# Kernel tuning notes

Measured on AMD Instinct MI355X. Metric: run time of the kernel, lower is better.

## Reference

```python
import jax, jax.numpy as jnp
import numpy as np

B, N, FIN, H, D = 4, 2048, 128, 4, 64
ALPHA = 0.2  # LeakyReLU negative slope


def _xavier_uniform(key, shape):
    fan_in, fan_out = shape[0], shape[1]
    limit = float(np.sqrt(6.0 / (fan_in + fan_out)))
    return jax.random.uniform(key, shape, jnp.float32, -limit, limit)


def setup_inputs() -> dict:
    key = jax.random.key(0)
    k1, k2, k3, k4 = jax.random.split(key, 4)
    x = jax.random.normal(k1, (B, N, FIN), jnp.float32)
    adj = jax.random.randint(k2, (B, N, N), 0, 2, jnp.int32)  # dense 0/1 mask
    W = _xavier_uniform(k3, (FIN, H * D))
    a = _xavier_uniform(k4, (2 * D, 1))
    return {"x": x, "adj": adj, "W": W, "a": a}


def reference(x, adj, W, a):
    Bb, Nn, _ = x.shape
    Dd = a.shape[0] // 2
    Hh = W.shape[1] // Dd
    # h: [B, N, H, D]
    h = (x @ W).reshape(Bb, Nn, Hh, Dd)
    # Additive attention: e[b,i,j,h] = leakyrelu(a1 . h[b,i,h] + a2 . h[b,j,h])
    a1 = a[:Dd, 0]
    a2 = a[Dd:, 0]
    ei = jnp.einsum('bnhd,d->bnh', h, a1)  # source (row i) term
    ej = jnp.einsum('bnhd,d->bnh', h, a2)  # dest (col j) term
    e = ei[:, :, None, :] + ej[:, None, :, :]  # [B, N, N, H]
    e = jnp.where(e >= 0, e, ALPHA * e)  # LeakyReLU
    e = jnp.where(adj[..., None] == 0, -jnp.inf, e)
    att = jax.nn.softmax(e, axis=2)  # softmax over neighbors j
    # dropout is a no-op in eval mode (training=False)
    out = jnp.einsum('bijh,bjhd->bihd', att, h)  # [B, N, H, D]
    return out.mean(axis=2)  # mean over heads -> [B, N, D]
```

## Files before the change

kernel.cpp:

```cpp
#include <hip/hip_runtime.h>

#define NN 2048
#define NH 4
#define DD 64
#define FIN 128
#define NB 4
#define LOG2E 1.44269504f

typedef unsigned short u16;
typedef unsigned int u32;
typedef short sh8 __attribute__((ext_vector_type(8)));
typedef float f32x4 __attribute__((ext_vector_type(4)));

static __device__ __forceinline__ u16 f2bf(float f) {
    u32 u = __builtin_bit_cast(u32, f);
    u += 0x7fffu + ((u >> 16) & 1u);
    return (u16)(u >> 16);
}
static __device__ __forceinline__ u32 pk_bf(float a, float b) {
    u32 ua = __builtin_bit_cast(u32, a) + 0x8000u;
    u32 ub = __builtin_bit_cast(u32, b) + 0x8000u;
    return __builtin_amdgcn_perm(ub, ua, 0x07060302u);
}
static __device__ __forceinline__ float fast_exp2(float x) {
    float r;
    asm("v_exp_f32 %0, %1" : "=v"(r) : "v"(x));
    return r;
}

static __device__ __forceinline__ void cd_probe(int ln15, int q, int* irow, int* icol) {
    sh8 pa, pb, qa, qb;
    #pragma unroll
    for (int ii = 0; ii < 8; ++ii) {
        pa[ii] = (short)f2bf((float)ln15);
        pb[ii] = 0;
        qa[ii] = 0;
        qb[ii] = (short)f2bf((float)ln15);
    }
    if (q == 0) { pb[0] = (short)f2bf(1.0f); qa[0] = (short)f2bf(1.0f); }
    f32x4 z = {};
    f32x4 prow = __builtin_amdgcn_mfma_f32_16x16x32_bf16(pa, pb, z, 0, 0, 0);
    f32x4 pcol = __builtin_amdgcn_mfma_f32_16x16x32_bf16(qa, qb, z, 0, 0, 0);
    #pragma unroll
    for (int r = 0; r < 4; ++r) {
        irow[r] = (int)(prow[r] + 0.5f);
        icol[r] = (int)(pcol[r] + 0.5f);
    }
}


__global__ __launch_bounds__(256)
void k_pack(const int* __restrict__ adj, const float* __restrict__ W,
            u32* __restrict__ msk, u16* __restrict__ WT) {
    const int tid = threadIdx.x;
    if (blockIdx.x < 2048) {
        const int wid  = (blockIdx.x * 256 + tid) >> 6;
        const int lane = tid & 63;
        for (int t0 = wid; t0 < NB * NN * 32; t0 += 32768) {
            int av[4];
            #pragma unroll
            for (int k = 0; k < 4; ++k) {
                const int t  = t0 + k * 8192;
                const int jc = t & 31;
                const int i  = (t >> 5) & (NN - 1);
                const int b  = t >> 16;
                av[k] = adj[((size_t)(b * NN + i)) * NN + jc * 64 + lane];
            }
            #pragma unroll
            for (int k = 0; k < 4; ++k) {
                const int t  = t0 + k * 8192;
                const int jc = t & 31;
                const int i  = (t >> 5) & (NN - 1);
                const int b  = t >> 16;
                const unsigned long long m = __ballot(av[k] != 0);
                if (lane == 0) {
                    msk[((size_t)(b * 64 + jc * 2 + 0)) * NN + i] = (u32)m;
                    msk[((size_t)(b * 64 + jc * 2 + 1)) * NN + i] = (u32)(m >> 32);
                }
            }
        }
    } else {
        const int bt  = blockIdx.x - 2048;
        const int kt  = bt & 3;
        const int ct8 = bt >> 2;
        __shared__ float tile[32][33];
        const int rr = tid >> 5, cc = tid & 31;
        #pragma unroll
        for (int i = 0; i < 4; ++i)
            tile[rr + 8 * i][cc] = W[(size_t)(kt * 32 + rr + 8 * i) * 256 + ct8 * 32 + cc];
        __syncthreads();
        #pragma unroll
        for (int i = 0; i < 4; ++i)
            WT[(size_t)(ct8 * 32 + rr + 8 * i) * FIN + kt * 32 + cc] = f2bf(tile[cc][rr + 8 * i]);
    }
}

__global__ __launch_bounds__(256)
void k_gemm_h(const float* __restrict__ x, const u16* __restrict__ WT,
              const float* __restrict__ a,
              u16* __restrict__ hT, float* __restrict__ ei_g, float* __restrict__ ej_g) {
    const int nb = blockIdx.x, b = blockIdx.y;
    const int tid = threadIdx.x, hd = tid >> 6, lane = tid & 63, ln15 = lane & 15, q = lane >> 4;
    const int q8 = q * 8;
    const int n0 = nb * 64;

    __shared__ u16 xs[64][136];
    __shared__ float cs[4][4][4][16][16];
    {
        const int col = (tid & 31) * 4;
        const int r0  = tid >> 5;
        #pragma unroll
        for (int rr = 0; rr < 8; ++rr) {
            const int row = r0 + rr * 8;
            const float4 v = *(const float4*)(x + ((size_t)(b * NN + n0 + row)) * FIN + col);
            *(u32*)&xs[row][col]     = pk_bf(v.x, v.y);
            *(u32*)&xs[row][col + 2] = pk_bf(v.z, v.w);
        }
    }
    __syncthreads();

    int irow[4], icol[4];
    cd_probe(ln15, q, irow, icol);

    f32x4 acc[4][4] = {};
    #pragma unroll
    for (int ks = 0; ks < 4; ++ks) {
        sh8 af[4], bfr[4];
        #pragma unroll
        for (int ct = 0; ct < 4; ++ct)
            af[ct] = *(const sh8*)(WT + (size_t)(hd * 64 + ct * 16 + ln15) * FIN + ks * 32 + q8);
        #pragma unroll
        for (int nt = 0; nt < 4; ++nt)
            bfr[nt] = *(const sh8*)&xs[nt * 16 + ln15][ks * 32 + q8];
        #pragma unroll
        for (int ct = 0; ct < 4; ++ct)
            #pragma unroll
            for (int nt = 0; nt < 4; ++nt)
                acc[ct][nt] = __builtin_amdgcn_mfma_f32_16x16x32_bf16(af[ct], bfr[nt], acc[ct][nt], 0, 0, 0);
    }

    float a1v[4][4], a2v[4][4];
    #pragma unroll
    for (int ct = 0; ct < 4; ++ct)
        #pragma unroll
        for (int r = 0; r < 4; ++r) {
            const int d = ct * 16 + 4 * q + r;
            a1v[ct][r] = a[d] * LOG2E;
            a2v[ct][r] = a[64 + d] * LOG2E;
        }

    float eip[4] = {}, ejq[4] = {};
    #pragma unroll
    for (int ct = 0; ct < 4; ++ct) {
        #pragma unroll
        for (int nt = 0; nt < 4; ++nt)
            #pragma unroll
            for (int r = 0; r < 4; ++r)
                cs[hd][ct][nt][irow[r]][icol[r]] = acc[ct][nt][r];
        #pragma unroll
        for (int nt = 0; nt < 4; ++nt) {
            #pragma unroll
            for (int r = 0; r < 4; ++r) {
                const float v = cs[hd][ct][nt][4 * q + r][ln15];
                const int d = ct * 16 + 4 * q + r;
                hT[((size_t)(b * 256 + hd * 64 + d)) * NN + n0 + nt * 16 + ln15] = f2bf(v);
                eip[nt] += v * a1v[ct][r];
                ejq[nt] += v * a2v[ct][r];
            }
        }
    }
    #pragma unroll
    for (int nt = 0; nt < 4; ++nt) {
        eip[nt] += __shfl_xor(eip[nt], 16);
        eip[nt] += __shfl_xor(eip[nt], 32);
        ejq[nt] += __shfl_xor(ejq[nt], 16);
        ejq[nt] += __shfl_xor(ejq[nt], 32);
    }
    if (lane < 16) {
        const size_t bhd = (size_t)(b * NH + hd) * NN;
        #pragma unroll
        for (int nt = 0; nt < 4; ++nt) {
            ei_g[bhd + n0 + nt * 16 + lane] = eip[nt];
            ej_g[bhd + n0 + nt * 16 + lane] = ejq[nt];
        }
    }
}

__global__ __launch_bounds__(256, 3)
void k_attn(const u32* __restrict__ msk, const u16* __restrict__ hT,
            const float* __restrict__ ei_g, const float* __restrict__ ej_g,
            float* __restrict__ o_part, float* __restrict__ l_part, int nj) {
    const int ib = blockIdx.x, js = blockIdx.y, b = blockIdx.z;
    const int js_n = gridDim.y;
    const int tid = threadIdx.x, hd = tid >> 6, lane = tid & 63, ln15 = lane & 15, q = lane >> 4;
    const int q8 = q * 8;
    const int iA = ib * 32 + ln15;

    int irow[4], icol[4];
    cd_probe(ln15, q, irow, icol);

    const size_t bhd = (size_t)(b * NH + hd) * NN;
    const float eivA = ei_g[bhd + iA];
    const float eivB = ei_g[bhd + iA + 16];
    const u32*   mptr = msk + (size_t)(b * 64) * NN;
    const float* ejp  = ej_g + bhd + q8;
    const u16*   hptr = hT + ((size_t)(b * 256 + hd * 64 + ln15)) * NN + q8;

    sh8 ones;
    #pragma unroll
    for (int ii = 0; ii < 8; ++ii) ones[ii] = (short)0x3F80;

    f32x4 acc[8] = {};
    f32x4 accl[2] = {};

    const int jt0 = js * nj;
    u32 mA = mptr[(size_t)jt0 * NN + iA];
    u32 mB = mptr[(size_t)jt0 * NN + iA + 16];
    float4 e0 = *(const float4*)(ejp + jt0 * 32);
    float4 e1 = *(const float4*)(ejp + jt0 * 32 + 4);
    sh8 h0 = *(const sh8*)(hptr + jt0 * 32);
    sh8 h1 = *(const sh8*)(hptr + 16 * NN + jt0 * 32);
    sh8 h2 = *(const sh8*)(hptr + 32 * NN + jt0 * 32);
    sh8 h3 = *(const sh8*)(hptr + 48 * NN + jt0 * 32);

    for (int t = 0; t < nj; ++t) {
        const int tn  = (t + 1 < nj) ? jt0 + t + 1 : jt0;
        const int jcn = tn * 32;
        const u32 mAn = mptr[(size_t)tn * NN + iA];
        const u32 mBn = mptr[(size_t)tn * NN + iA + 16];
        const float4 e0n = *(const float4*)(ejp + jcn);
        const float4 e1n = *(const float4*)(ejp + jcn + 4);
        const sh8 h0n = *(const sh8*)(hptr + jcn);
        const sh8 h1n = *(const sh8*)(hptr + 16 * NN + jcn);
        const sh8 h2n = *(const sh8*)(hptr + 32 * NN + jcn);
        const sh8 h3n = *(const sh8*)(hptr + 48 * NN + jcn);

        const float ef[8] = { e0.x, e0.y, e0.z, e0.w, e1.x, e1.y, e1.z, e1.w };
        const u32 mqA = mA >> q8;
        const u32 mqB = mB >> q8;
        float pA[8], pB[8];
        #pragma unroll
        for (int ii = 0; ii < 8; ++ii) {
            float eA = eivA + ef[ii];
            float eB = eivB + ef[ii];
            eA = fmaxf(eA, 0.2f * eA);
            eB = fmaxf(eB, 0.2f * eB);
            const float xA = fast_exp2(eA);
            const float xB = fast_exp2(eB);
            pA[ii] = (mqA & (1u << ii)) ? xA : 0.f;
            pB[ii] = (mqB & (1u << ii)) ? xB : 0.f;
        }
        union { uint4 u; sh8 v; } avA, avB;
        avA.u.x = pk_bf(pA[0], pA[1]); avA.u.y = pk_bf(pA[2], pA[3]);
        avA.u.z = pk_bf(pA[4], pA[5]); avA.u.w = pk_bf(pA[6], pA[7]);
        avB.u.x = pk_bf(pB[0], pB[1]); avB.u.y = pk_bf(pB[2], pB[3]);
        avB.u.z = pk_bf(pB[4], pB[5]); avB.u.w = pk_bf(pB[6], pB[7]);

        acc[0] = __builtin_amdgcn_mfma_f32_16x16x32_bf16(avA.v, h0, acc[0], 0, 0, 0);
        acc[1] = __builtin_amdgcn_mfma_f32_16x16x32_bf16(avA.v, h1, acc[1], 0, 0, 0);
        acc[2] = __builtin_amdgcn_mfma_f32_16x16x32_bf16(avA.v, h2, acc[2], 0, 0, 0);
        acc[3] = __builtin_amdgcn_mfma_f32_16x16x32_bf16(avA.v, h3, acc[3], 0, 0, 0);
        accl[0] = __builtin_amdgcn_mfma_f32_16x16x32_bf16(avA.v, ones, accl[0], 0, 0, 0);
        acc[4] = __builtin_amdgcn_mfma_f32_16x16x32_bf16(avB.v, h0, acc[4], 0, 0, 0);
        acc[5] = __builtin_amdgcn_mfma_f32_16x16x32_bf16(avB.v, h1, acc[5], 0, 0, 0);
        acc[6] = __builtin_amdgcn_mfma_f32_16x16x32_bf16(avB.v, h2, acc[6], 0, 0, 0);
        acc[7] = __builtin_amdgcn_mfma_f32_16x16x32_bf16(avB.v, h3, acc[7], 0, 0, 0);
        accl[1] = __builtin_amdgcn_mfma_f32_16x16x32_bf16(avB.v, ones, accl[1], 0, 0, 0);

        mA = mAn; mB = mBn; e0 = e0n; e1 = e1n;
        h0 = h0n; h1 = h1n; h2 = h2n; h3 = h3n;
    }

    const size_t pbA = (((size_t)b * 128 + ib * 2 + 0) * js_n + js) * NH + hd;
    const size_t pbB = (((size_t)b * 128 + ib * 2 + 1) * js_n + js) * NH + hd;
    #pragma unroll
    for (int r = 0; r < 4; ++r) {
        l_part[pbA * 16 + irow[r]] = accl[0][r];
        l_part[pbB * 16 + irow[r]] = accl[1][r];
    }
    float* opA = o_part + pbA * 1024;
    float* opB = o_part + pbB * 1024;
    #pragma unroll
    for (int dt = 0; dt < 4; ++dt)
        #pragma unroll
        for (int r = 0; r < 4; ++r) {
            opA[(size_t)irow[r] * 64 + dt * 16 + icol[r]] = acc[dt][r];
            opB[(size_t)irow[r] * 64 + dt * 16 + icol[r]] = acc[4 + dt][r];
        }
}

template <int JS>
__global__ __launch_bounds__(256)
void k_combine(const float* __restrict__ o_part, const float* __restrict__ l_part,
               float* __restrict__ out) {
    const int ib = blockIdx.x, b = blockIdx.y;
    const int tid = threadIdx.x;
    const int i = tid >> 4, d4 = (tid & 15) * 4;
    float  lv[NH][JS];
    float4 ov[NH][JS];
    #pragma unroll
    for (int h = 0; h < NH; ++h)
        #pragma unroll
        for (int js = 0; js < JS; ++js) {
            const size_t pbase = (((size_t)b * 128 + ib) * JS + js) * NH + h;
            lv[h][js] = l_part[pbase * 16 + i];
            ov[h][js] = *(const float4*)(o_part + pbase * 1024 + (size_t)i * 64 + d4);
        }
    float4 sacc = {0.f, 0.f, 0.f, 0.f};
    #pragma unroll
    for (int h = 0; h < NH; ++h) {
        float l = 0.f;
        float4 oh = {0.f, 0.f, 0.f, 0.f};
        #pragma unroll
        for (int js = 0; js < JS; ++js) {
            l += lv[h][js];
            oh.x += ov[h][js].x; oh.y += ov[h][js].y;
            oh.z += ov[h][js].z; oh.w += ov[h][js].w;
        }
        const float inv = 0.25f / l;
        sacc.x += oh.x * inv; sacc.y += oh.y * inv;
        sacc.z += oh.z * inv; sacc.w += oh.w * inv;
    }
    *(float4*)(out + ((size_t)(b * NN) + ib * 16 + i) * DD + d4) = sacc;
}

extern "C" void kernel_launch(void* const* d_in, const int* in_sizes, int n_in,
                              void* d_out, int out_size, void* d_ws, size_t ws_size,
                              hipStream_t stream) {
    const float* x = nullptr; const int* adj = nullptr;
    const float* W = nullptr; const float* a = nullptr;
    for (int i = 0; i < n_in; ++i) {
        switch (in_sizes[i]) {
            case NB * NN * FIN:  x   = (const float*)d_in[i]; break;
            case NB * NN * NN:   adj = (const int*)d_in[i];   break;
            case FIN * 256:      W   = (const float*)d_in[i]; break;
            case 2 * DD:         a   = (const float*)d_in[i]; break;
            default: break;
        }
    }
    if (!x)   x   = (const float*)d_in[0];
    if (!adj) adj = (const int*)d_in[1];
    if (!W)   W   = (const float*)d_in[2];
    if (!a)   a   = (const float*)d_in[3];
    float* out = (float*)d_out;

    char* ws = (char*)d_ws;
    u16*   WT  = (u16*)(ws);
    float* ei  = (float*)(ws + 65536);
    float* ej  = (float*)(ws + 196608);
    u16*   hT  = (u16*)(ws + 327680);
    u32*   msk = (u32*)(ws + 4521984);
    float* l_p = (float*)(ws + 6619136);
    float* o_p = (float*)(ws + 7143424);

    const size_t need4 = 7143424 + (size_t)4 * 8388608;
    const size_t need2 = 7143424 + (size_t)2 * 8388608;
    const int js_n = (ws_size >= need4) ? 4 : (ws_size >= need2) ? 2 : 1;

    k_pack<<<dim3(2080), dim3(256), 0, stream>>>(adj, W, msk, WT);
    k_gemm_h<<<dim3(32, NB), dim3(256), 0, stream>>>(x, WT, a, hT, ei, ej);
    k_attn<<<dim3(64, js_n, NB), dim3(256), 0, stream>>>(msk, hT, ei, ej, o_p, l_p, 64 / js_n);
    if (js_n == 4)      k_combine<4><<<dim3(128, NB), dim3(256), 0, stream>>>(o_p, l_p, out);
    else if (js_n == 2) k_combine<2><<<dim3(128, NB), dim3(256), 0, stream>>>(o_p, l_p, out);
    else                k_combine<1><<<dim3(128, NB), dim3(256), 0, stream>>>(o_p, l_p, out);
}
```

Before: 156.1 us.

## Pre-swizzle h into MFMA fragment layout and vectorize adjacency mask packing

The mask packer now reads adjacency as int4 per lane, builds nibbles and merges them with xor-shuffles, replacing the scalar loads and ballots per 64 columns. The GEMM kernel writes h in a fragment-ordered layout in which each lane's 8 bf16 values are contiguous, using 16-byte stores through a smaller padded LDS tile. The attention kernel then loads its B operands as fully coalesced contiguous 16-byte chunks instead of strided rows. This is meant to reduce adjacency read overhead and uncoalesced h traffic, at the cost of more complex indexing that must stay consistent between producer and consumer.

```diff
diff --git a/kernel.cpp b/kernel.cpp
--- a/kernel.cpp
+++ b/kernel.cpp
@@ -56,28 +56,18 @@
     if (blockIdx.x < 2048) {
         const int wid  = (blockIdx.x * 256 + tid) >> 6;
         const int lane = tid & 63;
-        for (int t0 = wid; t0 < NB * NN * 32; t0 += 32768) {
-            int av[4];
-            #pragma unroll
-            for (int k = 0; k < 4; ++k) {
-                const int t  = t0 + k * 8192;
-                const int jc = t & 31;
-                const int i  = (t >> 5) & (NN - 1);
-                const int b  = t >> 16;
-                av[k] = adj[((size_t)(b * NN + i)) * NN + jc * 64 + lane];
-            }
-            #pragma unroll
-            for (int k = 0; k < 4; ++k) {
-                const int t  = t0 + k * 8192;
-                const int jc = t & 31;
-                const int i  = (t >> 5) & (NN - 1);
-                const int b  = t >> 16;
-                const unsigned long long m = __ballot(av[k] != 0);
-                if (lane == 0) {
-                    msk[((size_t)(b * 64 + jc * 2 + 0)) * NN + i] = (u32)m;
-                    msk[((size_t)(b * 64 + jc * 2 + 1)) * NN + i] = (u32)(m >> 32);
-                }
-            }
+        for (int t = wid; t < NB * NN * 8; t += 8192) {
+            const int c256 = t & 7;
+            const int i    = (t >> 3) & (NN - 1);
+            const int b    = t >> 14;
+            const int4 v = *(const int4*)(adj + ((size_t)(b * NN + i)) * NN + c256 * 256 + lane * 4);
+            u32 nib = (v.x ? 1u : 0u) | (v.y ? 2u : 0u) | (v.z ? 4u : 0u) | (v.w ? 8u : 0u);
+            u32 w = nib << (4 * (lane & 7));
+            w |= __shfl_xor(w, 1);
+            w |= __shfl_xor(w, 2);
+            w |= __shfl_xor(w, 4);
+            if ((lane & 7) == 0)
+                msk[((size_t)(b * 64 + c256 * 8 + (lane >> 3))) * NN + i] = w;
         }
     } else {
         const int bt  = blockIdx.x - 2048;
@@ -98,14 +88,14 @@
 __global__ __launch_bounds__(256)
 void k_gemm_h(const float* __restrict__ x, const u16* __restrict__ WT,
               const float* __restrict__ a,
-              u16* __restrict__ hT, float* __restrict__ ei_g, float* __restrict__ ej_g) {
+              u16* __restrict__ hTf, float* __restrict__ ei_g, float* __restrict__ ej_g) {
     const int nb = blockIdx.x, b = blockIdx.y;
     const int tid = threadIdx.x, hd = tid >> 6, lane = tid & 63, ln15 = lane & 15, q = lane >> 4;
     const int q8 = q * 8;
     const int n0 = nb * 64;
 
     __shared__ u16 xs[64][136];
-    __shared__ float cs[4][4][4][16][16];
+    __shared__ float cs[NH][4][16][20];
     {
         const int col = (tid & 31) * 4;
         const int r0  = tid >> 5;
@@ -139,16 +129,6 @@
                 acc[ct][nt] = __builtin_amdgcn_mfma_f32_16x16x32_bf16(af[ct], bfr[nt], acc[ct][nt], 0, 0, 0);
     }
 
-    float a1v[4][4], a2v[4][4];
-    #pragma unroll
-    for (int ct = 0; ct < 4; ++ct)
-        #pragma unroll
-        for (int r = 0; r < 4; ++r) {
-            const int d = ct * 16 + 4 * q + r;
-            a1v[ct][r] = a[d] * LOG2E;
-            a2v[ct][r] = a[64 + d] * LOG2E;
-        }
-
     float eip[4] = {}, ejq[4] = {};
     #pragma unroll
     for (int ct = 0; ct < 4; ++ct) {
@@ -156,18 +136,33 @@
         for (int nt = 0; nt < 4; ++nt)
             #pragma unroll
             for (int r = 0; r < 4; ++r)
-                cs[hd][ct][nt][irow[r]][icol[r]] = acc[ct][nt][r];
-        #pragma unroll
-        for (int nt = 0; nt < 4; ++nt) {
+                cs[hd][nt][irow[r]][icol[r]] = acc[ct][nt][r];
+
+        #pragma unroll
+        for (int p = 0; p < 2; ++p) {
+            const float4 c0 = *(const float4*)&cs[hd][2 * p + (q >> 1)][ln15][(q & 1) * 8];
+            const float4 c1 = *(const float4*)&cs[hd][2 * p + (q >> 1)][ln15][(q & 1) * 8 + 4];
+            uint4 o;
+            o.x = pk_bf(c0.x, c0.y); o.y = pk_bf(c0.z, c0.w);
+            o.z = pk_bf(c1.x, c1.y); o.w = pk_bf(c1.z, c1.w);
+            *(uint4*)(hTf + ((((size_t)(b * NH + hd) * 64 + nb * 2 + p) * 4 + ct) * 512) + lane * 8) = o;
+        }
+
+        float a1v[4], a2v[4];
+        #pragma unroll
+        for (int r = 0; r < 4; ++r) {
+            const int d = ct * 16 + 4 * q + r;
+            a1v[r] = a[d] * LOG2E;
+            a2v[r] = a[64 + d] * LOG2E;
+        }
+        #pragma unroll
+        for (int nt = 0; nt < 4; ++nt)
             #pragma unroll
             for (int r = 0; r < 4; ++r) {
-                const float v = cs[hd][ct][nt][4 * q + r][ln15];
-                const int d = ct * 16 + 4 * q + r;
-                hT[((size_t)(b * 256 + hd * 64 + d)) * NN + n0 + nt * 16 + ln15] = f2bf(v);
-                eip[nt] += v * a1v[ct][r];
-                ejq[nt] += v * a2v[ct][r];
+                const float v = cs[hd][nt][4 * q + r][ln15];
+                eip[nt] += v * a1v[r];
+                ejq[nt] += v * a2v[r];
             }
-        }
     }
     #pragma unroll
     for (int nt = 0; nt < 4; ++nt) {
@@ -187,7 +182,7 @@
 }
 
 __global__ __launch_bounds__(256, 3)
-void k_attn(const u32* __restrict__ msk, const u16* __restrict__ hT,
+void k_attn(const u32* __restrict__ msk, const u16* __restrict__ hTf,
             const float* __restrict__ ei_g, const float* __restrict__ ej_g,
             float* __restrict__ o_part, float* __restrict__ l_part, int nj) {
     const int ib = blockIdx.x, js = blockIdx.y, b = blockIdx.z;
@@ -204,7 +199,7 @@
     const float eivB = ei_g[bhd + iA + 16];
     const u32*   mptr = msk + (size_t)(b * 64) * NN;
     const float* ejp  = ej_g + bhd + q8;
-    const u16*   hptr = hT + ((size_t)(b * 256 + hd * 64 + ln15)) * NN + q8;
+    const u16*   hfp  = hTf + (size_t)(b * NH + hd) * (64 * 2048) + (size_t)lane * 8;
 
     sh8 ones;
     #pragma unroll
@@ -218,22 +213,21 @@
     u32 mB = mptr[(size_t)jt0 * NN + iA + 16];
     float4 e0 = *(const float4*)(ejp + jt0 * 32);
     float4 e1 = *(const float4*)(ejp + jt0 * 32 + 4);
-    sh8 h0 = *(const sh8*)(hptr + jt0 * 32);
-    sh8 h1 = *(const sh8*)(hptr + 16 * NN + jt0 * 32);
-    sh8 h2 = *(const sh8*)(hptr + 32 * NN + jt0 * 32);
-    sh8 h3 = *(const sh8*)(hptr + 48 * NN + jt0 * 32);
+    sh8 h0 = *(const sh8*)(hfp + (size_t)jt0 * 2048);
+    sh8 h1 = *(const sh8*)(hfp + (size_t)jt0 * 2048 + 512);
+    sh8 h2 = *(const sh8*)(hfp + (size_t)jt0 * 2048 + 1024);
+    sh8 h3 = *(const sh8*)(hfp + (size_t)jt0 * 2048 + 1536);
 
     for (int t = 0; t < nj; ++t) {
-        const int tn  = (t + 1 < nj) ? jt0 + t + 1 : jt0;
-        const int jcn = tn * 32;
+        const int tn = (t + 1 < nj) ? jt0 + t + 1 : jt0;
         const u32 mAn = mptr[(size_t)tn * NN + iA];
         const u32 mBn = mptr[(size_t)tn * NN + iA + 16];
-        const float4 e0n = *(const float4*)(ejp + jcn);
-        const float4 e1n = *(const float4*)(ejp + jcn + 4);
-        const sh8 h0n = *(const sh8*)(hptr + jcn);
-        const sh8 h1n = *(const sh8*)(hptr + 16 * NN + jcn);
-        const sh8 h2n = *(const sh8*)(hptr + 32 * NN + jcn);
-        const sh8 h3n = *(const sh8*)(hptr + 48 * NN + jcn);
+        const float4 e0n = *(const float4*)(ejp + tn * 32);
+        const float4 e1n = *(const float4*)(ejp + tn * 32 + 4);
+        const sh8 h0n = *(const sh8*)(hfp + (size_t)tn * 2048);
+        const sh8 h1n = *(const sh8*)(hfp + (size_t)tn * 2048 + 512);
+        const sh8 h2n = *(const sh8*)(hfp + (size_t)tn * 2048 + 1024);
+        const sh8 h3n = *(const sh8*)(hfp + (size_t)tn * 2048 + 1536);
 
         const float ef[8] = { e0.x, e0.y, e0.z, e0.w, e1.x, e1.y, e1.z, e1.w };
         const u32 mqA = mA >> q8;
@@ -348,7 +342,7 @@
     u16*   WT  = (u16*)(ws);
     float* ei  = (float*)(ws + 65536);
     float* ej  = (float*)(ws + 196608);
-    u16*   hT  = (u16*)(ws + 327680);
+    u16*   hTf = (u16*)(ws + 327680);
     u32*   msk = (u32*)(ws + 4521984);
     float* l_p = (float*)(ws + 6619136);
     float* o_p = (float*)(ws + 7143424);
@@ -358,8 +352,8 @@
     const int js_n = (ws_size >= need4) ? 4 : (ws_size >= need2) ? 2 : 1;
 
     k_pack<<<dim3(2080), dim3(256), 0, stream>>>(adj, W, msk, WT);
-    k_gemm_h<<<dim3(32, NB), dim3(256), 0, stream>>>(x, WT, a, hT, ei, ej);
-    k_attn<<<dim3(64, js_n, NB), dim3(256), 0, stream>>>(msk, hT, ei, ej, o_p, l_p, 64 / js_n);
+    k_gemm_h<<<dim3(32, NB), dim3(256), 0, stream>>>(x, WT, a, hTf, ei, ej);
+    k_attn<<<dim3(64, js_n, NB), dim3(256), 0, stream>>>(msk, hTf, ei, ej, o_p, l_p, 64 / js_n);
     if (js_n == 4)      k_combine<4><<<dim3(128, NB), dim3(256), 0, stream>>>(o_p, l_p, out);
     else if (js_n == 2) k_combine<2><<<dim3(128, NB), dim3(256), 0, stream>>>(o_p, l_p, out);
     else                k_combine<1><<<dim3(128, NB), dim3(256), 0, stream>>>(o_p, l_p, out);
```

Result: faster. 146.4 us (-6.2%).
